# Optimization experiments

Hardware: AMD Instinct MI355X
Metric: run time of the kernel (lower is better)

## Reference

```python
import jax, jax.numpy as jnp
import numpy as np

B, T, D, L, H = 16, 2048, 512, 6, 1024  # batch, seq, embed_dim, num_layers, mlp hidden (2*D)
K = D // 2  # freq bands; k = min(D//2, T//2) = 256 here
VOCAB = 256


def _ln(x, g, b, eps=1e-5):
    m = x.mean(-1, keepdims=True)
    v = ((x - m) ** 2).mean(-1, keepdims=True)
    return (x - m) / jnp.sqrt(v + eps) * g + b


def setup_inputs() -> dict:
    key = jax.random.key(0)
    ks = jax.random.split(key, 12)
    s = 0.02
    return {
        "byte_ids": jax.random.randint(ks[0], (B, T), 0, 256),
        # ByteSpectralEmbedding params
        "freq_bands": jnp.ones((K,), jnp.float32),
        "fp_w1": jax.random.normal(ks[1], (D, 2 * D), jnp.float32) * s,
        "fp_b1": jnp.zeros((2 * D,), jnp.float32),
        "fp_ln_g": jnp.ones((2 * D,), jnp.float32),
        "fp_ln_b": jnp.zeros((2 * D,), jnp.float32),
        "fp_w2": jax.random.normal(ks[2], (2 * D, D), jnp.float32) * s,
        "fp_b2": jnp.zeros((D,), jnp.float32),
        # SpectralMLPBlock params, stacked over L layers (FNet-style spectral mixing + MLP)
        "blk_ln1_g": jnp.ones((L, D), jnp.float32),
        "blk_ln1_b": jnp.zeros((L, D), jnp.float32),
        "blk_ln2_g": jnp.ones((L, D), jnp.float32),
        "blk_ln2_b": jnp.zeros((L, D), jnp.float32),
        "blk_w1": jax.random.normal(ks[3], (L, D, H), jnp.float32) * s,
        "blk_b1": jnp.zeros((L, H), jnp.float32),
        "blk_w2": jax.random.normal(ks[4], (L, H, D), jnp.float32) * s,
        "blk_b2": jnp.zeros((L, D), jnp.float32),
        # final norm + output head
        "norm_g": jnp.ones((D,), jnp.float32),
        "norm_b": jnp.zeros((D,), jnp.float32),
        "out_w": jax.random.normal(ks[5], (D, VOCAB), jnp.float32) * s,
        "out_b": jnp.zeros((VOCAB,), jnp.float32),
    }


def reference(byte_ids, freq_bands, fp_w1, fp_b1, fp_ln_g, fp_ln_b, fp_w2, fp_b2,
              blk_ln1_g, blk_ln1_b, blk_ln2_g, blk_ln2_b, blk_w1, blk_b1, blk_w2, blk_b2,
              norm_g, norm_b, out_w, out_b):
    Bc, Tc = byte_ids.shape
    k = min(D // 2, Tc // 2)
    signal = byte_ids.astype(jnp.float32) / 127.5 - 1.0          # [B,T]
    X = jnp.fft.fft(signal, axis=1)[:, :k]                        # [B,k] single FFT
    # shift theorem: FFT(roll(signal, -p))[f] = X[f] * exp(+2pi i f p / T)
    mag = jnp.abs(X) * freq_bands[:k]                             # [B,k], position-independent
    base_phase = jnp.angle(X)                                     # [B,k]
    pos = jnp.arange(Tc, dtype=jnp.float32)
    f = jnp.arange(k, dtype=jnp.float32)
    phase = base_phase[:, None, :] + (2.0 * jnp.pi / Tc) * pos[None, :, None] * f[None, None, :]  # [B,T,k]
    mag_bt = jnp.broadcast_to(mag[:, None, :], (Bc, Tc, k))
    feats = jnp.concatenate([mag_bt, jnp.sin(phase), jnp.cos(phase)], axis=-1)
    feats = feats[..., :D] if feats.shape[-1] >= D else jnp.pad(feats, ((0, 0), (0, 0), (0, D - feats.shape[-1])))
    # freq_proj: Linear -> LayerNorm -> GELU -> Linear
    h = feats @ fp_w1 + fp_b1
    h = jax.nn.gelu(_ln(h, fp_ln_g, fp_ln_b), approximate=False)
    x = h @ fp_w2 + fp_b2                                         # [B,T,D]
    # SpectralMLPBlock stack: residual FFT mixing + residual MLP
    for i in range(L):
        y = _ln(x, blk_ln1_g[i], blk_ln1_b[i])
        x = x + jnp.fft.fft(jnp.fft.fft(y, axis=-1), axis=1).real
        y = _ln(x, blk_ln2_g[i], blk_ln2_b[i])
        x = x + jax.nn.gelu(y @ blk_w1[i] + blk_b1[i], approximate=False) @ blk_w2[i] + blk_b2[i]
    x = _ln(x, norm_g, norm_b)
    return x @ out_w + out_b                                      # [B,T,256]
```

## Files before the change

kernel.cpp:

```cpp
#include <hip/hip_runtime.h>
#include <cmath>

typedef unsigned short u16;
typedef unsigned int u32;

constexpr int NB = 16;
constexpr int NT = 2048;
constexpr int ND = 512;
constexpr int NL = 6;
constexpr int NH = 1024;
constexpr int NK = 256;
constexpr int NM = NB * NT;

constexpr float PI2 = 6.283185307179586f;

typedef short bf16x8 __attribute__((ext_vector_type(8)));
typedef float f32x4 __attribute__((ext_vector_type(4)));

__device__ __forceinline__ float gelu_exact(float v) {
    return 0.5f * v * (1.0f + erff(v * 0.70710678118654752f));
}

__device__ __forceinline__ u16 f2bf(float f) {
    union { float f; u32 u; } v; v.f = f;
    u32 r = v.u + 0x7FFFu + ((v.u >> 16) & 1u);
    return (u16)(r >> 16);
}

__device__ __forceinline__ float bf2f(u16 h) {
    union { u32 u; float f; } v; v.u = ((u32)h) << 16;
    return v.f;
}

__device__ __forceinline__ float block_sum256(float val, float* lds4) {
#pragma unroll
    for (int o = 32; o > 0; o >>= 1) val += __shfl_down(val, o);
    int lane = threadIdx.x & 63, wid = threadIdx.x >> 6;
    if (lane == 0) lds4[wid] = val;
    __syncthreads();
    float t = lds4[0] + lds4[1] + lds4[2] + lds4[3];
    __syncthreads();
    return t;
}

__device__ __forceinline__ void swz_block_t(int bm, int& row0, int& col0) {
    int nwg = gridDim.x * gridDim.y;
    int wg = blockIdx.x + blockIdx.y * gridDim.x;
    int L = wg;
    if ((nwg & 7) == 0) {
        int q = nwg >> 3;
        L = (wg & 7) * q + (wg >> 3);
    }
    int ncol = gridDim.y;
    row0 = (L / ncol) * bm;
    col0 = (L % ncol) * 128;
}

__global__ void twiddle_kernel(float2* __restrict__ tw) {
    int idx = blockIdx.x * 256 + threadIdx.x;
    if (idx < 2047) {
        u32 v = idx + 1;
        u32 h = 1u << (31 - __clz(v));
        u32 k = v - h;
        float a = -(float)M_PI * (float)k / (float)h;
        tw[idx] = make_float2(cosf(a), sinf(a));
    }
}

__global__ void dft_kernel(const int* __restrict__ bytes, const float* __restrict__ fb,
                           float* __restrict__ mag, float* __restrict__ cph,
                           float* __restrict__ sph) {
    __shared__ float lr[4], li[4];
    int b = blockIdx.x, f = blockIdx.y;
    float re = 0.f, im = 0.f;
    for (int t = threadIdx.x; t < NT; t += 256) {
        float s = (float)bytes[b * NT + t] * (1.0f / 127.5f) - 1.0f;
        int idx = (t * f) & (NT - 1);
        float a = (float)idx * (PI2 / NT);
        float sn, cs;
        sincosf(a, &sn, &cs);
        re += s * cs;
        im -= s * sn;
    }
#pragma unroll
    for (int o = 32; o > 0; o >>= 1) {
        re += __shfl_down(re, o);
        im += __shfl_down(im, o);
    }
    int lane = threadIdx.x & 63, wid = threadIdx.x >> 6;
    if (lane == 0) { lr[wid] = re; li[wid] = im; }
    __syncthreads();
    if (threadIdx.x == 0) {
        float R = lr[0] + lr[1] + lr[2] + lr[3];
        float I = li[0] + li[1] + li[2] + li[3];
        float m = sqrtf(R * R + I * I);
        mag[b * NK + f] = m * fb[f];
        float inv = (m > 0.f) ? 1.0f / m : 0.f;
        cph[b * NK + f] = (m > 0.f) ? R * inv : 1.0f;
        sph[b * NK + f] = I * inv;
    }
}

__global__ void feats_split_kernel(const float* __restrict__ mag,
                                   const float* __restrict__ cph,
                                   const float* __restrict__ sph,
                                   u16* __restrict__ hi, u16* __restrict__ lo) {
    int idx = blockIdx.x * 256 + threadIdx.x;
    int d = idx & (ND - 1);
    int m = idx >> 9;
    int b = m >> 11, t = m & (NT - 1);
    float v;
    if (d < NK) {
        v = mag[b * NK + d];
    } else {
        int f = d - NK;
        int a = (t * f) & (NT - 1);
        float sn, cs;
        sincosf((float)a * (PI2 / NT), &sn, &cs);
        v = sph[b * NK + f] * cs + cph[b * NK + f] * sn;
    }
    u16 h = f2bf(v);
    hi[idx] = h;
    lo[idx] = f2bf(v - bf2f(h));
}

template <int NV, int GELU, int OBF>
__global__ void ln_kernel(const float* __restrict__ in, const float* __restrict__ g,
                          const float* __restrict__ bta, void* __restrict__ outv) {
    __shared__ float lds4[4];
    constexpr int NE = NV / 256;
    size_t row = blockIdx.x;
    const float* p = in + row * NV;
    float v[NE];
    float sum = 0.f;
#pragma unroll
    for (int i = 0; i < NE; ++i) {
        v[i] = p[threadIdx.x + 256 * i];
        sum += v[i];
    }
    sum = block_sum256(sum, lds4);
    float mean = sum * (1.0f / NV);
    float sq = 0.f;
#pragma unroll
    for (int i = 0; i < NE; ++i) {
        float d = v[i] - mean;
        sq += d * d;
    }
    sq = block_sum256(sq, lds4);
    float inv = rsqrtf(sq * (1.0f / NV) + 1e-5f);
#pragma unroll
    for (int i = 0; i < NE; ++i) {
        int c = threadIdx.x + 256 * i;
        float r = (v[i] - mean) * inv * g[c] + bta[c];
        if (GELU) r = gelu_exact(r);
        if (OBF == 2) {
            u16* o = (u16*)outv + row * (2 * NV);
            u16 hb = f2bf(r);
            o[c] = hb;
            o[NV + c] = f2bf(r - bf2f(hb));
        } else if (OBF == 1) {
            ((u16*)outv)[row * NV + c] = f2bf(r);
        } else {
            ((float*)outv)[row * NV + c] = r;
        }
    }
}

__global__ void ln_fftd_kernel(const float* __restrict__ x, const float* __restrict__ g,
                               const float* __restrict__ bta, float* __restrict__ P,
                               const float2* __restrict__ twid) {
    __shared__ float sr[4][512], si[4][512];
    int wv = threadIdx.x >> 6, lane = threadIdx.x & 63;
    int rlocal = blockIdx.x * 4 + wv;
    const float* p = x + (size_t)rlocal * ND;
    float v[8];
    float s = 0.f;
#pragma unroll
    for (int j = 0; j < 8; ++j) { v[j] = p[lane + 64 * j]; s += v[j]; }
#pragma unroll
    for (int o = 32; o > 0; o >>= 1) s += __shfl_down(s, o);
    s = __shfl(s, 0);
    float mean = s * (1.0f / ND);
    float q = 0.f;
#pragma unroll
    for (int j = 0; j < 8; ++j) { float d = v[j] - mean; q += d * d; }
#pragma unroll
    for (int o = 32; o > 0; o >>= 1) q += __shfl_down(q, o);
    q = __shfl(q, 0);
    float inv = rsqrtf(q * (1.0f / ND) + 1e-5f);
#pragma unroll
    for (int j = 0; j < 8; ++j) {
        int i = lane + 64 * j;
        int r = __brev((unsigned)i) >> 23;
        sr[wv][r] = (v[j] - mean) * inv * g[i] + bta[i];
        si[wv][r] = 0.f;
    }
    for (int len = 2; len <= 512; len <<= 1) {
        int half = len >> 1;
#pragma unroll
        for (int qq = lane; qq < 256; qq += 64) {
            int k = qq & (half - 1);
            int j = ((qq - k) << 1) + k;
            float2 tw = twid[(half - 1) + k];
            float cs = tw.x, sn = tw.y;
            float ur = sr[wv][j], ui = si[wv][j];
            float vr = sr[wv][j + half], vi = si[wv][j + half];
            float tr = vr * cs - vi * sn;
            float ti = vr * sn + vi * cs;
            sr[wv][j] = ur + tr;
            si[wv][j] = ui + ti;
            sr[wv][j + half] = ur - tr;
            si[wv][j + half] = ui - ti;
        }
    }
    float* out = P + (size_t)rlocal * ND;
#pragma unroll
    for (int j = 0; j < 8; ++j) {
        int i = lane + 64 * j;
        out[i] = (i <= 256) ? sr[wv][i] : si[wv][i - 256];
    }
}

__global__ void transpose_bt_kernel(const float* __restrict__ P, float* __restrict__ PT) {
    __shared__ float tile[32][33];
    int b = blockIdx.z, t0 = blockIdx.x * 32, d0 = blockIdx.y * 32;
    int j = threadIdx.x & 31, i0 = threadIdx.x >> 5;
    for (int i = i0; i < 32; i += 8)
        tile[i][j] = P[((size_t)(b * NT + t0 + i)) * ND + d0 + j];
    __syncthreads();
    for (int i = i0; i < 32; i += 8)
        PT[((size_t)(b * ND + d0 + i)) * NT + t0 + j] = tile[j][i];
}

__global__ void fft_t2048_kernel(const float* __restrict__ PT, float* __restrict__ Mt,
                                 const float2* __restrict__ twid) {
    __shared__ float sr[2048], si[2048];
    int b = blockIdx.x;
    int d = blockIdx.y;
    const float* zr = PT + ((size_t)(b * ND + d)) * NT;
    const float* zi = PT + ((size_t)(b * ND + 256 + d)) * NT;
    bool has_im = (d != 0) && (d != 256);
    for (int t = threadIdx.x; t < 2048; t += 256) {
        int r = __brev((unsigned)t) >> 21;
        sr[r] = zr[t];
        si[r] = has_im ? zi[t] : 0.f;
    }
    __syncthreads();
    for (int len = 2; len <= 2048; len <<= 1) {
        int half = len >> 1;
        for (int q = threadIdx.x; q < 1024; q += 256) {
            int k = q & (half - 1);
            int j = ((q - k) << 1) + k;
            float2 tw = twid[(half - 1) + k];
            float cs = tw.x, sn = tw.y;
            float ur = sr[j], ui = si[j];
            float vr = sr[j + half], vi = si[j + half];
            float tr = vr * cs - vi * sn;
            float ti = vr * sn + vi * cs;
            sr[j] = ur + tr;
            si[j] = ui + ti;
            sr[j + half] = ur - tr;
            si[j + half] = ui - ti;
        }
        __syncthreads();
    }
    float* m0 = Mt + ((size_t)(b * ND + d)) * NT;
    for (int t = threadIdx.x; t < 2048; t += 256) m0[t] = sr[t];
    if (has_im) {
        float* m1 = Mt + ((size_t)(b * ND + (512 - d))) * NT;
        for (int t = threadIdx.x; t < 2048; t += 256) m1[t] = sr[(2048 - t) & 2047];
    }
}

__global__ void addt_ln_kernel(const float* __restrict__ Mt, float* __restrict__ x,
                               const float* __restrict__ g, const float* __restrict__ bta,
                               u16* __restrict__ yb) {
    __shared__ float tile[512 * 17];
    int b = blockIdx.y, t0 = blockIdx.x * 16;
    int tid = threadIdx.x;
    for (int lin = tid; lin < 512 * 16; lin += 256) {
        int tloc = lin & 15, d = lin >> 4;
        tile[d * 17 + tloc] = Mt[((size_t)(b * ND + d)) * NT + t0 + tloc];
    }
    __syncthreads();
    int lane = tid & 63, wv = tid >> 6;
#pragma unroll
    for (int rr = 0; rr < 4; ++rr) {
        int tloc = wv * 4 + rr;
        size_t row = (size_t)(b * NT + t0 + tloc);
        float v[8];
        float s = 0.f;
#pragma unroll
        for (int e = 0; e < 8; ++e) {
            int d = lane + 64 * e;
            v[e] = x[row * ND + d] + tile[d * 17 + tloc];
            s += v[e];
        }
#pragma unroll
        for (int o = 32; o > 0; o >>= 1) s += __shfl_down(s, o);
        s = __shfl(s, 0);
        float mean = s * (1.0f / ND);
        float q = 0.f;
#pragma unroll
        for (int e = 0; e < 8; ++e) { float d2 = v[e] - mean; q += d2 * d2; }
#pragma unroll
        for (int o = 32; o > 0; o >>= 1) q += __shfl_down(q, o);
        q = __shfl(q, 0);
        float inv = rsqrtf(q * (1.0f / ND) + 1e-5f);
#pragma unroll
        for (int e = 0; e < 8; ++e) {
            int d = lane + 64 * e;
            x[row * ND + d] = v[e];
            yb[row * ND + d] = f2bf((v[e] - mean) * inv * g[d] + bta[d]);
        }
    }
}

__global__ void wconv_kernel(const float* __restrict__ W, u16* __restrict__ Wt,
                             int K, int N) {
    __shared__ float tile[32][33];
    size_t moff = (size_t)blockIdx.z * K * N;
    int n0 = blockIdx.x * 32, k0 = blockIdx.y * 32;
    int j = threadIdx.x & 31, i0 = threadIdx.x >> 5;
    for (int i = i0; i < 32; i += 8)
        tile[i][j] = W[moff + (size_t)(k0 + i) * N + n0 + j];
    __syncthreads();
    for (int i = i0; i < 32; i += 8)
        Wt[moff + (size_t)(n0 + i) * K + k0 + j] = f2bf(tile[j][i]);
}

template <int GELU, int ACC, int OBF, int ADDB>
__global__ __launch_bounds__(512) void mfma_gemm(
    const u16* __restrict__ A, int lda, const u16* __restrict__ Wt,
    const float* __restrict__ bias, void* __restrict__ Cv, int Kd, int Nd) {
    __shared__ __align__(16) u16 Al[2][8192];
    __shared__ __align__(16) u16 Bl[2][4096];
    int tid = threadIdx.x;
    int row0, col0;
    swz_block_t(256, row0, col0);
    int lane = tid & 63, w = tid >> 6;
    int wr = w >> 1, wc = w & 1;
    int kg = lane >> 4, ln16 = lane & 15;

    f32x4 acc[4][4] = {};

    auto stage = [&](int buf, int t) {
        int k0 = t << 5;
#pragma unroll
        for (int i = 0; i < 2; ++i) {
            int s = i * 512 + tid;
            int skg = s >> 8, r = s & 255;
            const u16* ga = A + (size_t)(row0 + r) * lda + k0 + skg * 8;
            __builtin_amdgcn_global_load_lds(
                (const __attribute__((address_space(1))) void*)ga,
                (__attribute__((address_space(3))) void*)&Al[buf][s * 8], 16, 0, 0);
        }
        {
            int s = tid;
            int skg = s >> 7, r = s & 127;
            const u16* gb = Wt + (size_t)(col0 + r) * Kd + k0 + skg * 8;
            __builtin_amdgcn_global_load_lds(
                (const __attribute__((address_space(1))) void*)gb,
                (__attribute__((address_space(3))) void*)&Bl[buf][s * 8], 16, 0, 0);
        }
    };
    auto compute = [&](int buf) {
        bf16x8 af[4], bfr[4];
#pragma unroll
        for (int mi = 0; mi < 4; ++mi)
            af[mi] = *(const bf16x8*)&Al[buf][(kg * 256 + wr * 64 + mi * 16 + ln16) * 8];
#pragma unroll
        for (int ni = 0; ni < 4; ++ni)
            bfr[ni] = *(const bf16x8*)&Bl[buf][(kg * 128 + wc * 64 + ni * 16 + ln16) * 8];
#pragma unroll
        for (int mi = 0; mi < 4; ++mi)
#pragma unroll
            for (int ni = 0; ni < 4; ++ni)
                acc[mi][ni] = __builtin_amdgcn_mfma_f32_16x16x32_bf16(
                    af[mi], bfr[ni], acc[mi][ni], 0, 0, 0);
    };

    int nt = Kd >> 5;
    stage(0, 0);
    __syncthreads();
    int cur = 0;
    for (int t = 1; t < nt; ++t) {
        stage(cur ^ 1, t);
        compute(cur);
        __syncthreads();
        cur ^= 1;
    }
    compute(cur);

#pragma unroll
    for (int mi = 0; mi < 4; ++mi) {
#pragma unroll
        for (int ni = 0; ni < 4; ++ni) {
            int col = col0 + wc * 64 + ni * 16 + ln16;
            float bv = ADDB ? bias[col] : 0.f;
#pragma unroll
            for (int j = 0; j < 4; ++j) {
                int row = row0 + wr * 64 + mi * 16 + kg * 4 + j;
                float v = acc[mi][ni][j] + bv;
                if (GELU) v = gelu_exact(v);
                size_t o = (size_t)row * Nd + col;
                if (OBF) {
                    ((u16*)Cv)[o] = f2bf(v);
                } else {
                    float* C = (float*)Cv;
                    if (ACC) v += C[o];
                    C[o] = v;
                }
            }
        }
    }
}

__global__ __launch_bounds__(256) void mfma_gemm2(
    const u16* __restrict__ Ahi, const u16* __restrict__ Alo, int lda,
    const u16* __restrict__ Wt, const float* __restrict__ bias,
    float* __restrict__ C, int Kd, int Nd) {
    __shared__ __align__(16) u16 Ah[3][4096];
    __shared__ __align__(16) u16 Al2[3][4096];
    __shared__ __align__(16) u16 Bl[3][4096];
    int tid = threadIdx.x;
    int row0, col0;
    swz_block_t(128, row0, col0);
    int lane = tid & 63, w = tid >> 6;
    int wr = w >> 1, wc = w & 1;
    int kg = lane >> 4, ln16 = lane & 15;

    f32x4 acc[4][4] = {};

    auto stage = [&](int buf, int t) {
        int k0 = t << 5;
#pragma unroll
        for (int i = 0; i < 2; ++i) {
            int s = i * 256 + tid;
            int skg = s >> 7, r = s & 127;
            size_t aoff = (size_t)(row0 + r) * lda + k0 + skg * 8;
            __builtin_amdgcn_global_load_lds(
                (const __attribute__((address_space(1))) void*)(Ahi + aoff),
                (__attribute__((address_space(3))) void*)&Ah[buf][s * 8], 16, 0, 0);
            __builtin_amdgcn_global_load_lds(
                (const __attribute__((address_space(1))) void*)(Alo + aoff),
                (__attribute__((address_space(3))) void*)&Al2[buf][s * 8], 16, 0, 0);
            const u16* gb = Wt + (size_t)(col0 + r) * Kd + k0 + skg * 8;
            __builtin_amdgcn_global_load_lds(
                (const __attribute__((address_space(1))) void*)gb,
                (__attribute__((address_space(3))) void*)&Bl[buf][s * 8], 16, 0, 0);
        }
    };
    auto compute = [&](int buf) {
        bf16x8 ah[4], al[4], bfr[4];
#pragma unroll
        for (int mi = 0; mi < 4; ++mi) {
            int sl = (kg * 128 + wr * 64 + mi * 16 + ln16) * 8;
            ah[mi] = *(const bf16x8*)&Ah[buf][sl];
            al[mi] = *(const bf16x8*)&Al2[buf][sl];
        }
#pragma unroll
        for (int ni = 0; ni < 4; ++ni)
            bfr[ni] = *(const bf16x8*)&Bl[buf][(kg * 128 + wc * 64 + ni * 16 + ln16) * 8];
#pragma unroll
        for (int mi = 0; mi < 4; ++mi)
#pragma unroll
            for (int ni = 0; ni < 4; ++ni) {
                acc[mi][ni] = __builtin_amdgcn_mfma_f32_16x16x32_bf16(
                    ah[mi], bfr[ni], acc[mi][ni], 0, 0, 0);
                acc[mi][ni] = __builtin_amdgcn_mfma_f32_16x16x32_bf16(
                    al[mi], bfr[ni], acc[mi][ni], 0, 0, 0);
            }
    };

    int nt = Kd >> 5;
    stage(0, 0);
    stage(1, 1);
    for (int t = 0; t < nt; ++t) {
        if (t + 1 < nt) asm volatile("s_waitcnt vmcnt(6)" ::: "memory");
        else            asm volatile("s_waitcnt vmcnt(0)" ::: "memory");
        __builtin_amdgcn_sched_barrier(0);
        __builtin_amdgcn_s_barrier();
        __builtin_amdgcn_sched_barrier(0);
        if (t + 2 < nt) stage((t + 2) % 3, t + 2);
        compute(t % 3);
    }

#pragma unroll
    for (int mi = 0; mi < 4; ++mi) {
#pragma unroll
        for (int ni = 0; ni < 4; ++ni) {
            int col = col0 + wc * 64 + ni * 16 + ln16;
            float bv = bias[col];
#pragma unroll
            for (int j = 0; j < 4; ++j) {
                int row = row0 + wr * 64 + mi * 16 + kg * 4 + j;
                C[(size_t)row * Nd + col] = acc[mi][ni][j] + bv;
            }
        }
    }
}

extern "C" void kernel_launch(void* const* d_in, const int* in_sizes, int n_in,
                              void* d_out, int out_size, void* d_ws, size_t ws_size,
                              hipStream_t stream) {
    const int* byte_ids     = (const int*)d_in[0];
    const float* freq_bands = (const float*)d_in[1];
    const float* fp_w1   = (const float*)d_in[2];
    const float* fp_b1   = (const float*)d_in[3];
    const float* fp_ln_g = (const float*)d_in[4];
    const float* fp_ln_b = (const float*)d_in[5];
    const float* fp_w2   = (const float*)d_in[6];
    const float* fp_b2   = (const float*)d_in[7];
    const float* blk_ln1_g = (const float*)d_in[8];
    const float* blk_ln1_b = (const float*)d_in[9];
    const float* blk_ln2_g = (const float*)d_in[10];
    const float* blk_ln2_b = (const float*)d_in[11];
    const float* blk_w1  = (const float*)d_in[12];
    const float* blk_b1  = (const float*)d_in[13];
    const float* blk_w2  = (const float*)d_in[14];
    const float* blk_b2  = (const float*)d_in[15];
    const float* norm_g  = (const float*)d_in[16];
    const float* norm_b  = (const float*)d_in[17];
    const float* out_w   = (const float*)d_in[18];
    const float* out_b   = (const float*)d_in[19];
    float* out = (float*)d_out;
    char* base = (char*)d_ws;
    char* obase = (char*)d_out;
    const size_t MB = 1048576;

    u16* fhi     = (u16*)base;
    u16* flo     = (u16*)(base + 32 * MB);
    float* xA    = (float*)base;
    float* hfp   = (float*)(base + 64 * MB);
    u16* h2      = (u16*)hfp;
    float* Zbuf  = (float*)(base + 64 * MB);
    float* PTbuf = (float*)(base + 128 * MB);
    float* Mtbuf = Zbuf;
    u16* hmlp    = (u16*)(base + 64 * MB);
    u16* ybf     = (u16*)(base + 128 * MB);
    u16* outwt   = (u16*)(base + 64 * MB);
    u16* fpw1t   = (u16*)obase;
    u16* fpw2t   = (u16*)(obase + 1 * MB);
    float* mag   = (float*)(obase + 2 * MB);
    float* cph   = mag + NB * NK;
    float* sph   = cph + NB * NK;
    float2* twid = (float2*)(obase + 4 * MB);
    u16* blkw1t  = (u16*)(obase + 6 * MB);
    u16* blkw2t  = (u16*)(obase + 12 * MB);

    twiddle_kernel<<<8, 256, 0, stream>>>(twid);

    dft_kernel<<<dim3(NB, NK), 256, 0, stream>>>(byte_ids, freq_bands, mag, cph, sph);
    feats_split_kernel<<<(NM * ND) / 256, 256, 0, stream>>>(mag, cph, sph, fhi, flo);
    wconv_kernel<<<dim3(NH / 32, ND / 32, 1), 256, 0, stream>>>(fp_w1, fpw1t, ND, NH);
    wconv_kernel<<<dim3(ND / 32, NH / 32, 1), 256, 0, stream>>>(fp_w2, fpw2t, NH, ND);
    wconv_kernel<<<dim3(NH / 32, ND / 32, NL), 256, 0, stream>>>(blk_w1, blkw1t, ND, NH);
    wconv_kernel<<<dim3(ND / 32, NH / 32, NL), 256, 0, stream>>>(blk_w2, blkw2t, NH, ND);

    mfma_gemm2<<<dim3(NM / 128, NH / 128), 256, 0, stream>>>(
        fhi, flo, ND, fpw1t, fp_b1, hfp, ND, NH);
    ln_kernel<NH, 1, 2><<<NM, 256, 0, stream>>>(hfp, fp_ln_g, fp_ln_b, h2);
    mfma_gemm2<<<dim3(NM / 128, ND / 128), 256, 0, stream>>>(
        h2, h2 + NH, 2 * NH, fpw2t, fp_b2, xA, NH, ND);

    for (int l = 0; l < NL; ++l) {
        ln_fftd_kernel<<<NM / 4, 256, 0, stream>>>(
            xA, blk_ln1_g + l * ND, blk_ln1_b + l * ND, Zbuf, twid);
        transpose_bt_kernel<<<dim3(NT / 32, ND / 32, NB), 256, 0, stream>>>(Zbuf, PTbuf);
        fft_t2048_kernel<<<dim3(NB, 257), 256, 0, stream>>>(PTbuf, Mtbuf, twid);
        addt_ln_kernel<<<dim3(NT / 16, NB), 256, 0, stream>>>(
            Mtbuf, xA, blk_ln2_g + l * ND, blk_ln2_b + l * ND, ybf);
        mfma_gemm<1, 0, 1, 1><<<dim3(NM / 256, NH / 128), 512, 0, stream>>>(
            ybf, ND, blkw1t + (size_t)l * ND * NH, blk_b1 + l * NH, hmlp, ND, NH);
        mfma_gemm<0, 1, 0, 1><<<dim3(NM / 256, ND / 128), 512, 0, stream>>>(
            hmlp, NH, blkw2t + (size_t)l * ND * NH, blk_b2 + l * ND, xA, NH, ND);
    }

    ln_kernel<ND, 0, 1><<<NM, 256, 0, stream>>>(xA, norm_g, norm_b, ybf);
    wconv_kernel<<<dim3(256 / 32, ND / 32, 1), 256, 0, stream>>>(out_w, outwt, ND, 256);
    mfma_gemm<0, 0, 0, 1><<<dim3(NM / 256, 256 / 128), 512, 0, stream>>>(
        ybf, ND, outwt, out_b, out, ND, 256);
}
```

Before: 2.729 ms.

## Fuse transpose into T-axis FFT with strided direct loads and swizzled block mapping

Removes the separate transpose kernel and its intermediate buffer. The T-axis FFT now reads columns straight from the row-major buffer with stride ND. The 1D grid is remapped so that concurrently scheduled workgroups cover adjacent d columns and share cache lines. Workspace buffers are rearranged to fit the new layout. This saves a full read and write pass per layer, but each workgroup's loads become strided and uncoalesced, so performance depends on how well the L2 and MALL absorb that traffic.

```diff
diff --git a/kernel.cpp b/kernel.cpp
--- a/kernel.cpp
+++ b/kernel.cpp
@@ -221,29 +221,21 @@
     }
 }
 
-__global__ void transpose_bt_kernel(const float* __restrict__ P, float* __restrict__ PT) {
-    __shared__ float tile[32][33];
-    int b = blockIdx.z, t0 = blockIdx.x * 32, d0 = blockIdx.y * 32;
-    int j = threadIdx.x & 31, i0 = threadIdx.x >> 5;
-    for (int i = i0; i < 32; i += 8)
-        tile[i][j] = P[((size_t)(b * NT + t0 + i)) * ND + d0 + j];
-    __syncthreads();
-    for (int i = i0; i < 32; i += 8)
-        PT[((size_t)(b * ND + d0 + i)) * NT + t0 + j] = tile[j][i];
-}
-
-__global__ void fft_t2048_kernel(const float* __restrict__ PT, float* __restrict__ Mt,
-                                 const float2* __restrict__ twid) {
+__global__ void fftt_direct_kernel(const float* __restrict__ P, float* __restrict__ Mt,
+                                   const float2* __restrict__ twid) {
     __shared__ float sr[2048], si[2048];
-    int b = blockIdx.x;
-    int d = blockIdx.y;
-    const float* zr = PT + ((size_t)(b * ND + d)) * NT;
-    const float* zi = PT + ((size_t)(b * ND + 256 + d)) * NT;
+    int wg = blockIdx.x;
+    int x = wg & 7, p = wg >> 3;
+    int b, d;
+    if (p < 512) { d = x * 32 + (p & 31); b = p >> 5; }
+    else         { d = 256; b = x * 2 + (p - 512); }
+    const float* pr = P + (size_t)b * NT * ND + d;
+    const float* pi = P + (size_t)b * NT * ND + 256 + d;
     bool has_im = (d != 0) && (d != 256);
     for (int t = threadIdx.x; t < 2048; t += 256) {
         int r = __brev((unsigned)t) >> 21;
-        sr[r] = zr[t];
-        si[r] = has_im ? zi[t] : 0.f;
+        sr[r] = pr[(size_t)t * ND];
+        si[r] = has_im ? pi[(size_t)t * ND] : 0.f;
     }
     __syncthreads();
     for (int len = 2; len <= 2048; len <<= 1) {
@@ -534,12 +526,11 @@
     float* xA    = (float*)base;
     float* hfp   = (float*)(base + 64 * MB);
     u16* h2      = (u16*)hfp;
-    float* Zbuf  = (float*)(base + 64 * MB);
-    float* PTbuf = (float*)(base + 128 * MB);
-    float* Mtbuf = Zbuf;
-    u16* hmlp    = (u16*)(base + 64 * MB);
-    u16* ybf     = (u16*)(base + 128 * MB);
-    u16* outwt   = (u16*)(base + 64 * MB);
+    float* Pbuf  = (float*)(base + 64 * MB);
+    float* Mtbuf = (float*)(base + 128 * MB);
+    u16* ybf     = (u16*)(base + 64 * MB);
+    u16* hmlp    = (u16*)(base + 96 * MB);
+    u16* outwt   = (u16*)(base + 96 * MB);
     u16* fpw1t   = (u16*)obase;
     u16* fpw2t   = (u16*)(obase + 1 * MB);
     float* mag   = (float*)(obase + 2 * MB);
@@ -566,9 +557,8 @@
 
     for (int l = 0; l < NL; ++l) {
         ln_fftd_kernel<<<NM / 4, 256, 0, stream>>>(
-            xA, blk_ln1_g + l * ND, blk_ln1_b + l * ND, Zbuf, twid);
-        transpose_bt_kernel<<<dim3(NT / 32, ND / 32, NB), 256, 0, stream>>>(Zbuf, PTbuf);
-        fft_t2048_kernel<<<dim3(NB, 257), 256, 0, stream>>>(PTbuf, Mtbuf, twid);
+            xA, blk_ln1_g + l * ND, blk_ln1_b + l * ND, Pbuf, twid);
+        fftt_direct_kernel<<<4112, 256, 0, stream>>>(Pbuf, Mtbuf, twid);
         addt_ln_kernel<<<dim3(NT / 16, NB), 256, 0, stream>>>(
             Mtbuf, xA, blk_ln2_g + l * ND, blk_ln2_b + l * ND, ybf);
         mfma_gemm<1, 0, 1, 1><<<dim3(NM / 256, NH / 128), 512, 0, stream>>>(
```

Result: no change. 2.711 ms (-0.7%).
